# Kernel optimization log

Hardware: AMD Instinct MI355X
Metric: run time of the kernel (lower is better)

## Reference

```python
import jax, jax.numpy as jnp
import numpy as np

B, S, D, H, KD, VD, HID, L, V, OUTN = 16, 512, 512, 8, 64, 64, 2048, 4, 32000, 128
EPS = 1e-5


def _layer_norm(x, g, b):
    m = jnp.mean(x, axis=-1, keepdims=True)
    v = jnp.mean(jnp.square(x - m), axis=-1, keepdims=True)
    return (x - m) * jax.lax.rsqrt(v + EPS) * g + b


def _pos_encoding(seq_len, d_model):
    pos = jnp.arange(seq_len, dtype=jnp.float32)[:, None]
    div = jnp.exp(jnp.arange(0, d_model, 2, dtype=jnp.float32) * (-np.log(10000.0) / d_model))
    pe = jnp.zeros((seq_len, d_model), dtype=jnp.float32)
    pe = pe.at[:, 0::2].set(jnp.sin(pos * div))
    pe = pe.at[:, 1::2].set(jnp.cos(pos * div))
    return pe


def setup_inputs() -> dict:
    key = jax.random.key(0)
    ks = jax.random.split(key, 32)
    s = 0.02
    n = jax.random.normal
    inp = {
        "enc_inputs": jax.random.randint(ks[0], (B, S), 0, V, dtype=jnp.int32),
        "emb": n(ks[1], (V, D), jnp.float32) * s,
        # stacked per-layer params, leading dim = L
        "Wq": n(ks[2], (L, D, H * KD), jnp.float32) * s,
        "bq": jnp.zeros((L, H * KD), jnp.float32),
        "Wk": n(ks[3], (L, D, H * KD), jnp.float32) * s,
        "bk": jnp.zeros((L, H * KD), jnp.float32),
        "Wv": n(ks[4], (L, D, H * VD), jnp.float32) * s,
        "bv": jnp.zeros((L, H * VD), jnp.float32),
        "Wo": n(ks[5], (L, H * VD, D), jnp.float32) * s,
        "bo": jnp.zeros((L, D), jnp.float32),
        "ln1_g": jnp.ones((L, D), jnp.float32),
        "ln1_b": jnp.zeros((L, D), jnp.float32),
        "W1": n(ks[6], (L, D, HID), jnp.float32) * s,   # conv1d k=1 == linear
        "b1": jnp.zeros((L, HID), jnp.float32),
        "W2": n(ks[7], (L, HID, D), jnp.float32) * s,
        "b2": jnp.zeros((L, D), jnp.float32),
        "ln2_g": jnp.ones((L, D), jnp.float32),
        "ln2_b": jnp.zeros((L, D), jnp.float32),
        # flatten head created inside torch forward: [S*D, 128]
        "Wf": n(ks[8], (S * D, OUTN), jnp.float32) * s,
        "bf": jnp.zeros((OUTN,), jnp.float32),
        "Wout": n(ks[9], (OUTN, 1), jnp.float32) * s,
        "bout": jnp.zeros((1,), jnp.float32),
    }
    return inp


def _encoder(enc_inputs, emb, Wq, bq, Wk, bk, Wv, bv, Wo, bo, ln1_g, ln1_b,
             W1, b1, W2, b2, ln2_g, ln2_b, Wf, bf, Wout, bout):
    x = emb[enc_inputs] + _pos_encoding(S, D)[None, :, :]          # [B,S,D]
    pad = (enc_inputs == 0)[:, None, None, :]                      # [B,1,1,S]
    scale = 1.0 / np.sqrt(D)                                       # note: sqrt(embed_dim), as in source
    for l in range(L):
        # multi-head attention
        q = (x @ Wq[l] + bq[l]).reshape(B, S, H, KD)
        k = (x @ Wk[l] + bk[l]).reshape(B, S, H, KD)
        v = (x @ Wv[l] + bv[l]).reshape(B, S, H, VD)
        scores = jnp.einsum('bqhd,bkhd->bhqk', q, k) * scale
        scores = jnp.where(pad, -1e9, scores)
        attn = jax.nn.softmax(scores, axis=-1)
        ctx = jnp.einsum('bhqk,bkhd->bqhd', attn, v).reshape(B, S, H * VD)
        x = _layer_norm(ctx @ Wo[l] + bo[l] + x, ln1_g[l], ln1_b[l])
        # position-wise FFN (conv1d kernel_size=1)
        h = jax.nn.relu(x @ W1[l] + b1[l])
        x = _layer_norm(h @ W2[l] + b2[l] + x, ln2_g[l], ln2_b[l])
    flat = x.reshape(B, S * D)
    features = flat @ Wf + bf                                      # [B,128]
    y_score = jax.nn.sigmoid(features @ Wout + bout)               # [B,1]
    y_pred = jnp.round(y_score)
    return y_score, y_pred, features


def reference(enc_inputs, emb, Wq, bq, Wk, bk, Wv, bv, Wo, bo, ln1_g, ln1_b,
              W1, b1, W2, b2, ln2_g, ln2_b, Wf, bf, Wout, bout):
    return _encoder(enc_inputs, emb, Wq, bq, Wk, bk, Wv, bv, Wo, bo, ln1_g, ln1_b,
                    W1, b1, W2, b2, ln2_g, ln2_b, Wf, bf, Wout, bout)
```

## Files before the change

### kernel.cpp

```cpp
#include <hip/hip_runtime.h>
#include <hip/hip_bf16.h>
#include <math.h>

typedef unsigned short ushort_t;
typedef __attribute__((ext_vector_type(8))) short bf16x8;
typedef __attribute__((ext_vector_type(4))) float f32x4;

#define SCALE_QK 0.04419417382415922f
#define PE_C 0.017988946039015986f

__device__ __forceinline__ void g2lds16(const void* g, void* l) {
    __builtin_amdgcn_global_load_lds(
        (const __attribute__((address_space(1))) unsigned int*)g,
        (__attribute__((address_space(3))) unsigned int*)l,
        16, 0, 0);
}
__device__ __forceinline__ ushort_t f2bs(float v) {
    __hip_bfloat16 h = __float2bfloat16(v);
    return *reinterpret_cast<ushort_t*>(&h);
}
__device__ __forceinline__ float bs2f(ushort_t v) {
    return __uint_as_float(((unsigned int)v) << 16);
}

template<bool RELU, bool VT>
__global__ __launch_bounds__(512, 2) void gemm8(
    const ushort_t* __restrict__ A, const ushort_t* __restrict__ B,
    const float* __restrict__ bias, ushort_t* __restrict__ C,
    ushort_t* __restrict__ vt, int K, int lda, int ldb, int ldc)
{
    __shared__ ushort_t As[2][256 * 64];
    __shared__ ushort_t Bs[2][256 * 64];

    const int t = threadIdx.x;
    const int lane = t & 63, w = t >> 6;
    const int l16 = lane & 15, quad = lane >> 4;
    const int r8 = lane >> 3;
    const int kg = ((lane & 7) ^ r8) << 3;
    const int wm = (w >> 2) * 128;
    const int wn = (w & 3) * 64;
    const int m0 = blockIdx.y * 256, n0 = blockIdx.x * 256;
    const int NT = K >> 6;

    f32x4 acc[8][4];
    #pragma unroll
    for (int i = 0; i < 8; i++)
        #pragma unroll
        for (int j = 0; j < 4; j++)
            acc[i][j] = (f32x4){0.f, 0.f, 0.f, 0.f};

    auto STAGE8 = [&](int kt, int bb) {
        int k0 = kt << 6;
        #pragma unroll
        for (int ii = 0; ii < 4; ii++) {
            int rbase = w * 32 + ii * 8;
            g2lds16(A + (size_t)(m0 + rbase + r8) * lda + k0 + kg,
                    &As[bb][rbase * 64]);
            g2lds16(B + (size_t)(n0 + rbase + r8) * ldb + k0 + kg,
                    &Bs[bb][rbase * 64]);
        }
    };

    STAGE8(0, 0);
    STAGE8(1, 1);

    for (int kt = 0; kt < NT; kt++) {
        const int bb = kt & 1;
        if (kt < NT - 1)
            asm volatile("s_waitcnt vmcnt(8)" ::: "memory");
        else
            asm volatile("s_waitcnt vmcnt(0)" ::: "memory");
        __builtin_amdgcn_s_barrier();
        asm volatile("" ::: "memory");

        #pragma unroll
        for (int tt = 0; tt < 2; tt++) {
            bf16x8 af[8], bf[4];
            #pragma unroll
            for (int i = 0; i < 8; i++) {
                int row = wm + i * 16 + l16;
                af[i] = *(const bf16x8*)&As[bb][row * 64 + ((((tt << 2) + quad) ^ (row & 7)) << 3)];
            }
            #pragma unroll
            for (int j = 0; j < 4; j++) {
                int row = wn + j * 16 + l16;
                bf[j] = *(const bf16x8*)&Bs[bb][row * 64 + ((((tt << 2) + quad) ^ (row & 7)) << 3)];
            }
            #pragma unroll
            for (int i = 0; i < 8; i++)
                #pragma unroll
                for (int j = 0; j < 4; j++)
                    acc[i][j] = __builtin_amdgcn_mfma_f32_16x16x32_bf16(
                        af[i], bf[j], acc[i][j], 0, 0, 0);
        }

        asm volatile("" ::: "memory");
        __builtin_amdgcn_s_barrier();
        asm volatile("" ::: "memory");
        if (kt + 2 < NT)
            STAGE8(kt + 2, bb);
    }

    if (VT && n0 >= 1024) {
        #pragma unroll
        for (int i = 0; i < 8; i++) {
            int mbase = m0 + wm + i * 16 + quad * 4;
            int b = mbase >> 9, s = mbase & 511;
            #pragma unroll
            for (int j = 0; j < 4; j++) {
                int n = n0 + wn + j * 16 + l16;
                int hv = n - 1024;
                int h = hv >> 6, vd = hv & 63;
                float bv = bias[n];
                ushort4 pk;
                pk.x = f2bs(acc[i][j][0] + bv);
                pk.y = f2bs(acc[i][j][1] + bv);
                pk.z = f2bs(acc[i][j][2] + bv);
                pk.w = f2bs(acc[i][j][3] + bv);
                *(ushort4*)&vt[((size_t)((b << 3) + h)) * 32768 + (size_t)vd * 512 + s] = pk;
            }
        }
        return;
    }

    #pragma unroll
    for (int i = 0; i < 8; i++)
        #pragma unroll
        for (int j = 0; j < 4; j++) {
            int n = n0 + wn + j * 16 + l16;
            float bv = bias[n];
            #pragma unroll
            for (int r = 0; r < 4; r++) {
                int m = m0 + wm + i * 16 + quad * 4 + r;
                float v = acc[i][j][r] + bv;
                if (RELU) v = fmaxf(v, 0.f);
                C[(size_t)m * ldc + n] = f2bs(v);
            }
        }
}

__global__ __launch_bounds__(512) void gemmLN(
    const ushort_t* __restrict__ A, const ushort_t* __restrict__ B,
    const float* __restrict__ bias, const ushort_t* __restrict__ res,
    const float* __restrict__ g, const float* __restrict__ bt,
    ushort_t* __restrict__ X, int K, int lda)
{
    __shared__ ushort_t As[2][32 * 64];
    __shared__ ushort_t Bs[2][512 * 64];
    __shared__ float2 pst[8][32];
    __shared__ float2 rmv[32];

    const int t = threadIdx.x;
    const int lane = t & 63, w = t >> 6;
    const int l16 = lane & 15, quad = lane >> 4;
    const int r8 = lane >> 3;
    const int kg = ((lane & 7) ^ r8) << 3;
    const int wn = w * 64;
    const int m0 = blockIdx.x * 32;
    const int NT = K >> 6;

    f32x4 acc[2][4];
    #pragma unroll
    for (int i = 0; i < 2; i++)
        #pragma unroll
        for (int j = 0; j < 4; j++)
            acc[i][j] = (f32x4){0.f, 0.f, 0.f, 0.f};

    auto STAGE = [&](int kt, int bb) {
        int k0 = kt << 6;
        if (w < 4)
            g2lds16(A + (size_t)(m0 + w * 8 + r8) * lda + k0 + kg,
                    &As[bb][(w * 8) * 64]);
        #pragma unroll
        for (int ii = 0; ii < 8; ii++) {
            int rbase = w * 64 + ii * 8;
            g2lds16(B + (size_t)(rbase + r8) * K + k0 + kg,
                    &Bs[bb][rbase * 64]);
        }
    };

    STAGE(0, 0);
    STAGE(1, 1);

    for (int kt = 0; kt < NT; kt++) {
        const int bb = kt & 1;
        if (kt < NT - 1) {
            if (w < 4) asm volatile("s_waitcnt vmcnt(9)" ::: "memory");
            else       asm volatile("s_waitcnt vmcnt(8)" ::: "memory");
        } else {
            asm volatile("s_waitcnt vmcnt(0)" ::: "memory");
        }
        __builtin_amdgcn_s_barrier();
        asm volatile("" ::: "memory");

        #pragma unroll
        for (int tt = 0; tt < 2; tt++) {
            bf16x8 af[2], bf4[4];
            #pragma unroll
            for (int i = 0; i < 2; i++) {
                int row = i * 16 + l16;
                af[i] = *(const bf16x8*)&As[bb][row * 64 + ((((tt << 2) + quad) ^ (row & 7)) << 3)];
            }
            #pragma unroll
            for (int j = 0; j < 4; j++) {
                int row = wn + j * 16 + l16;
                bf4[j] = *(const bf16x8*)&Bs[bb][row * 64 + ((((tt << 2) + quad) ^ (row & 7)) << 3)];
            }
            #pragma unroll
            for (int i = 0; i < 2; i++)
                #pragma unroll
                for (int j = 0; j < 4; j++)
                    acc[i][j] = __builtin_amdgcn_mfma_f32_16x16x32_bf16(
                        af[i], bf4[j], acc[i][j], 0, 0, 0);
        }

        asm volatile("" ::: "memory");
        __builtin_amdgcn_s_barrier();
        asm volatile("" ::: "memory");
        if (kt + 2 < NT)
            STAGE(kt + 2, bb);
    }

    float rs[2][4], rq[2][4];
    #pragma unroll
    for (int i = 0; i < 2; i++)
        #pragma unroll
        for (int r = 0; r < 4; r++) { rs[i][r] = 0.f; rq[i][r] = 0.f; }

    #pragma unroll
    for (int i = 0; i < 2; i++)
        #pragma unroll
        for (int j = 0; j < 4; j++) {
            int n = wn + j * 16 + l16;
            float bvn = bias[n];
            #pragma unroll
            for (int r = 0; r < 4; r++) {
                int row = i * 16 + quad * 4 + r;
                float v = acc[i][j][r] + bvn
                        + bs2f(res[(size_t)(m0 + row) * 512 + n]);
                acc[i][j][r] = v;
                rs[i][r] += v;
                rq[i][r] += v * v;
            }
        }

    #pragma unroll
    for (int i = 0; i < 2; i++)
        #pragma unroll
        for (int r = 0; r < 4; r++) {
            #pragma unroll
            for (int off = 1; off < 16; off <<= 1) {
                rs[i][r] += __shfl_xor(rs[i][r], off);
                rq[i][r] += __shfl_xor(rq[i][r], off);
            }
            if (l16 == 0)
                pst[w][i * 16 + quad * 4 + r] = make_float2(rs[i][r], rq[i][r]);
        }
    __syncthreads();
    if (t < 32) {
        float s = 0.f, q = 0.f;
        #pragma unroll
        for (int wv = 0; wv < 8; wv++) {
            float2 p = pst[wv][t];
            s += p.x; q += p.y;
        }
        float mean = s * (1.f / 512.f);
        float var = q * (1.f / 512.f) - mean * mean;
        rmv[t] = make_float2(mean, rsqrtf(var + 1e-5f));
    }
    __syncthreads();

    #pragma unroll
    for (int i = 0; i < 2; i++)
        #pragma unroll
        for (int j = 0; j < 4; j++) {
            int n = wn + j * 16 + l16;
            float gn = g[n], btn = bt[n];
            #pragma unroll
            for (int r = 0; r < 4; r++) {
                int row = i * 16 + quad * 4 + r;
                float2 mr = rmv[row];
                float o = (acc[i][j][r] - mr.x) * mr.y * gn + btn;
                X[(size_t)(m0 + row) * 512 + n] = f2bs(o);
            }
        }
}

__global__ __launch_bounds__(256) void flash_attn(
    ushort_t* __restrict__ QKV, const ushort_t* __restrict__ Vt,
    const int* __restrict__ tok)
{
    __shared__ ushort_t Qs[128 * 64];
    __shared__ ushort_t Ks[128 * 64];
    __shared__ ushort_t Vts[64 * 128];
    __shared__ ushort_t Ps[128 * 128];

    const int bh = blockIdx.y;
    const int b = bh >> 3, h = bh & 7;
    const int q0 = blockIdx.x * 128;
    const int t = threadIdx.x;
    const int lane = t & 63, w = t >> 6;
    const int l16 = lane & 15, quad = lane >> 4;
    const int wm = w * 32;
    const size_t rowbase = (size_t)b * 512;

    {
        int r8 = lane >> 3;
        int kg = (lane & 7) ^ r8;
        #pragma unroll
        for (int ii = 0; ii < 4; ii++) {
            int rb = w * 32 + ii * 8;
            g2lds16(QKV + (rowbase + q0 + rb + r8) * 1536 + h * 64 + kg * 8,
                    &Qs[rb * 64]);
        }
    }

    f32x4 accO[2][4];
    #pragma unroll
    for (int i = 0; i < 2; i++)
        #pragma unroll
        for (int jv = 0; jv < 4; jv++)
            accO[i][jv] = (f32x4){0.f, 0.f, 0.f, 0.f};
    float lrow[2][4];
    #pragma unroll
    for (int i = 0; i < 2; i++)
        #pragma unroll
        for (int r = 0; r < 4; r++) lrow[i][r] = 0.f;

    for (int kc = 0; kc < 4; kc++) {
        __syncthreads();
        {
            int r8 = lane >> 3;
            int kg = (lane & 7) ^ r8;
            #pragma unroll
            for (int ii = 0; ii < 4; ii++) {
                int rb = w * 32 + ii * 8;
                g2lds16(QKV + (rowbase + kc * 128 + rb + r8) * 1536 + 512 + h * 64 + kg * 8,
                        &Ks[rb * 64]);
            }
        }
        {
            int v4 = lane >> 4;
            #pragma unroll
            for (int ii = 0; ii < 4; ii++) {
                int vb = w * 16 + ii * 4;
                int vd = vb + v4;
                int kg = (lane & 15) ^ (vd & 15);
                g2lds16(Vt + (size_t)bh * 32768 + (size_t)vd * 512 + kc * 128 + kg * 8,
                        &Vts[vb * 128]);
            }
        }
        float maskv[8];
        #pragma unroll
        for (int j = 0; j < 8; j++)
            maskv[j] = (tok[b * 512 + kc * 128 + j * 16 + l16] == 0) ? -1e9f : 0.f;

        __syncthreads();

        f32x4 sacc[2][8];
        #pragma unroll
        for (int i = 0; i < 2; i++)
            #pragma unroll
            for (int j = 0; j < 8; j++)
                sacc[i][j] = (f32x4){0.f, 0.f, 0.f, 0.f};
        #pragma unroll
        for (int tt = 0; tt < 2; tt++) {
            bf16x8 aq[2], bk8[8];
            #pragma unroll
            for (int i = 0; i < 2; i++) {
                int row = wm + i * 16 + l16;
                aq[i] = *(const bf16x8*)&Qs[row * 64 + (((tt << 2) + quad) ^ (row & 7)) * 8];
            }
            #pragma unroll
            for (int j = 0; j < 8; j++) {
                int row = j * 16 + l16;
                bk8[j] = *(const bf16x8*)&Ks[row * 64 + (((tt << 2) + quad) ^ (row & 7)) * 8];
            }
            #pragma unroll
            for (int i = 0; i < 2; i++)
                #pragma unroll
                for (int j = 0; j < 8; j++)
                    sacc[i][j] = __builtin_amdgcn_mfma_f32_16x16x32_bf16(
                        aq[i], bk8[j], sacc[i][j], 0, 0, 0);
        }

        #pragma unroll
        for (int i = 0; i < 2; i++)
            #pragma unroll
            for (int j = 0; j < 8; j++)
                #pragma unroll
                for (int r = 0; r < 4; r++) {
                    float p = __expf(fmaf(sacc[i][j][r], SCALE_QK, maskv[j]));
                    sacc[i][j][r] = p;
                    lrow[i][r] += p;
                }

        #pragma unroll
        for (int i = 0; i < 2; i++)
            #pragma unroll
            for (int j = 0; j < 8; j++) {
                int col = j * 16 + l16;
                int colc = col >> 3, csub = col & 7;
                #pragma unroll
                for (int r = 0; r < 4; r++) {
                    int row = wm + i * 16 + quad * 4 + r;
                    Ps[row * 128 + ((colc ^ (row & 15)) << 3) + csub] = f2bs(sacc[i][j][r]);
                }
            }

        #pragma unroll
        for (int tt = 0; tt < 4; tt++) {
            bf16x8 ap[2], bv8[4];
            #pragma unroll
            for (int i = 0; i < 2; i++) {
                int row = wm + i * 16 + l16;
                ap[i] = *(const bf16x8*)&Ps[row * 128 + ((((tt << 2) + quad)) ^ (row & 15)) * 8];
            }
            #pragma unroll
            for (int jv = 0; jv < 4; jv++) {
                int vd = jv * 16 + l16;
                bv8[jv] = *(const bf16x8*)&Vts[vd * 128 + (((tt << 2) + quad) ^ (vd & 15)) * 8];
            }
            #pragma unroll
            for (int i = 0; i < 2; i++)
                #pragma unroll
                for (int jv = 0; jv < 4; jv++)
                    accO[i][jv] = __builtin_amdgcn_mfma_f32_16x16x32_bf16(
                        ap[i], bv8[jv], accO[i][jv], 0, 0, 0);
        }
    }

    #pragma unroll
    for (int i = 0; i < 2; i++)
        #pragma unroll
        for (int r = 0; r < 4; r++) {
            float s = lrow[i][r];
            #pragma unroll
            for (int off = 1; off < 16; off <<= 1)
                s += __shfl_xor(s, off);
            float inv = 1.f / s;
            int row = q0 + wm + i * 16 + quad * 4 + r;
            #pragma unroll
            for (int jv = 0; jv < 4; jv++) {
                int vd = jv * 16 + l16;
                QKV[(rowbase + row) * 1536 + h * 64 + vd] = f2bs(accO[i][jv][r] * inv);
            }
        }
}

__global__ __launch_bounds__(256) void prep(
    const float* __restrict__ Wq, const float* __restrict__ Wk,
    const float* __restrict__ Wv, const float* __restrict__ Wo,
    const float* __restrict__ W1, const float* __restrict__ W2,
    const float* __restrict__ bq, const float* __restrict__ bk,
    const float* __restrict__ bv, const int* __restrict__ tok,
    const float* __restrict__ emb,
    __hip_bfloat16* __restrict__ WqkvT, __hip_bfloat16* __restrict__ WoT,
    __hip_bfloat16* __restrict__ W1T, __hip_bfloat16* __restrict__ W2T,
    float* __restrict__ bqkv, float* __restrict__ Fb,
    __hip_bfloat16* __restrict__ xb)
{
    const int blk = blockIdx.x;
    const int t = threadIdx.x;

    if (blk < 12288) {
        __shared__ float tile[32][33];
        const float* in; __hip_bfloat16* out;
        long long inz, outz; int R, Cc, bx, by, bz;
        if (blk < 4096) {
            int seg = blk >> 10, lb = blk & 1023;
            bz = lb >> 8; by = (lb >> 4) & 15; bx = lb & 15;
            R = 512; Cc = 512; inz = 262144;
            if      (seg == 0) { in = Wq; out = WqkvT;          outz = 786432; }
            else if (seg == 1) { in = Wk; out = WqkvT + 262144; outz = 786432; }
            else if (seg == 2) { in = Wv; out = WqkvT + 524288; outz = 786432; }
            else               { in = Wo; out = WoT;            outz = 262144; }
        } else if (blk < 8192) {
            int lb = blk - 4096;
            bz = lb >> 10; by = (lb >> 6) & 15; bx = lb & 63;
            R = 512; Cc = 2048; inz = 1048576; outz = 1048576;
            in = W1; out = W1T;
        } else {
            int lb = blk - 8192;
            bz = lb >> 10; by = (lb >> 4) & 63; bx = lb & 15;
            R = 2048; Cc = 512; inz = 1048576; outz = 1048576;
            in = W2; out = W2T;
        }
        in += bz * inz; out += bz * outz;
        int c0 = bx * 32, r0 = by * 32;
        int tx = t & 31, ty = t >> 5;
        #pragma unroll
        for (int i = 0; i < 4; i++)
            tile[ty + i * 8][tx] = in[(size_t)(r0 + ty + i * 8) * Cc + c0 + tx];
        __syncthreads();
        #pragma unroll
        for (int i = 0; i < 4; i++)
            out[(size_t)(c0 + ty + i * 8) * R + r0 + tx] =
                __float2bfloat16(tile[tx][ty + i * 8]);
    } else if (blk < 12312) {
        int k = blk - 12288;
        int idx = k * 256 + t;
        int l = idx / 1536, n = idx - l * 1536;
        float v = (n < 512) ? bq[l * 512 + n]
                : (n < 1024) ? bk[l * 512 + n - 512]
                             : bv[l * 512 + n - 1024];
        bqkv[idx] = v;
        if (k < 8) Fb[k * 256 + t] = 0.f;
    } else {
        int idx = (blk - 12312) * 256 + t;
        int d  = idx & 511;
        int bs = idx >> 9;
        int s  = bs & 511;
        int tk = tok[bs];
        float freq  = expf(-(float)(d & ~1) * PE_C);
        float angle = (float)s * freq;
        float pe    = (d & 1) ? cosf(angle) : sinf(angle);
        xb[idx] = __float2bfloat16(emb[(size_t)tk * 512 + d] + pe);
    }
}

__global__ __launch_bounds__(256) void feat_partial(const ushort_t* __restrict__ Xb,
                                                    const float* __restrict__ Wf,
                                                    float* __restrict__ Fb) {
    const int slice = blockIdx.x;
    const int k0 = slice * 128;
    __shared__ float Xs[16][128];
    __shared__ float Red[2048];
    const int t = threadIdx.x;

    #pragma unroll
    for (int i = 0; i < 2; i++) {
        int idx = t + i * 256;
        int b = idx >> 5, c4 = (idx & 31) * 4;
        ushort4 u = *(const ushort4*)&Xb[(size_t)b * 262144 + k0 + c4];
        Xs[b][c4 + 0] = bs2f(u.x);
        Xs[b][c4 + 1] = bs2f(u.y);
        Xs[b][c4 + 2] = bs2f(u.z);
        Xs[b][c4 + 3] = bs2f(u.w);
    }
    #pragma unroll
    for (int i = 0; i < 8; i++) Red[t + i * 256] = 0.f;
    __syncthreads();

    const int n4 = (t & 31) * 4;
    const int kh = t >> 5;
    const int rbase = kh * 16;
    const float* wp = Wf + (size_t)(k0 + rbase) * 128 + n4;

    float4 acc[16];
    #pragma unroll
    for (int b = 0; b < 16; b++) acc[b] = (float4){0.f, 0.f, 0.f, 0.f};

    #pragma unroll
    for (int half = 0; half < 2; half++) {
        float4 wv[8];
        #pragma unroll
        for (int kk = 0; kk < 8; kk++)
            wv[kk] = *(const float4*)&wp[(size_t)(half * 8 + kk) * 128];
        #pragma unroll
        for (int b = 0; b < 16; b++) {
            float4 x0 = *(const float4*)&Xs[b][rbase + half * 8];
            float4 x1 = *(const float4*)&Xs[b][rbase + half * 8 + 4];
            acc[b].x += x0.x*wv[0].x + x0.y*wv[1].x + x0.z*wv[2].x + x0.w*wv[3].x
                      + x1.x*wv[4].x + x1.y*wv[5].x + x1.z*wv[6].x + x1.w*wv[7].x;
            acc[b].y += x0.x*wv[0].y + x0.y*wv[1].y + x0.z*wv[2].y + x0.w*wv[3].y
                      + x1.x*wv[4].y + x1.y*wv[5].y + x1.z*wv[6].y + x1.w*wv[7].y;
            acc[b].z += x0.x*wv[0].z + x0.y*wv[1].z + x0.z*wv[2].z + x0.w*wv[3].z
                      + x1.x*wv[4].z + x1.y*wv[5].z + x1.z*wv[6].z + x1.w*wv[7].z;
            acc[b].w += x0.x*wv[0].w + x0.y*wv[1].w + x0.z*wv[2].w + x0.w*wv[3].w
                      + x1.x*wv[4].w + x1.y*wv[5].w + x1.z*wv[6].w + x1.w*wv[7].w;
        }
    }

    #pragma unroll
    for (int b = 0; b < 16; b++) {
        atomicAdd(&Red[b * 128 + n4 + 0], acc[b].x);
        atomicAdd(&Red[b * 128 + n4 + 1], acc[b].y);
        atomicAdd(&Red[b * 128 + n4 + 2], acc[b].z);
        atomicAdd(&Red[b * 128 + n4 + 3], acc[b].w);
    }
    __syncthreads();
    #pragma unroll
    for (int i = 0; i < 8; i++) {
        int o = t + i * 256;
        atomicAdd(&Fb[o], Red[o]);
    }
}

__global__ __launch_bounds__(256) void head_kernel(const float* __restrict__ feat,
                                                   const float* __restrict__ bfv,
                                                   const float* __restrict__ Wo2,
                                                   const float* __restrict__ bo2,
                                                   float* __restrict__ out) {
    __shared__ float f[2048];
    int t = threadIdx.x;
    for (int i = t; i < 2048; i += 256) {
        float v = feat[i] + bfv[i & 127];
        f[i] = v;
        out[32 + i] = v;
    }
    __syncthreads();
    if (t < 16) {
        float zv = bo2[0];
        for (int n = 0; n < 128; n++) zv = fmaf(f[t * 128 + n], Wo2[n], zv);
        float ys = 1.f / (1.f + expf(-zv));
        out[t] = ys;
        out[16 + t] = rintf(ys);
    }
}

extern "C" void kernel_launch(void* const* d_in, const int* in_sizes, int n_in,
                              void* d_out, int out_size, void* d_ws, size_t ws_size,
                              hipStream_t stream) {
    const int*   enc  = (const int*)  d_in[0];
    const float* emb  = (const float*)d_in[1];
    const float* Wq   = (const float*)d_in[2];
    const float* bq   = (const float*)d_in[3];
    const float* Wk   = (const float*)d_in[4];
    const float* bk   = (const float*)d_in[5];
    const float* Wv   = (const float*)d_in[6];
    const float* bv   = (const float*)d_in[7];
    const float* Wo   = (const float*)d_in[8];
    const float* bo   = (const float*)d_in[9];
    const float* g1   = (const float*)d_in[10];
    const float* be1  = (const float*)d_in[11];
    const float* W1   = (const float*)d_in[12];
    const float* b1f  = (const float*)d_in[13];
    const float* W2   = (const float*)d_in[14];
    const float* b2f  = (const float*)d_in[15];
    const float* g2   = (const float*)d_in[16];
    const float* be2  = (const float*)d_in[17];
    const float* Wf   = (const float*)d_in[18];
    const float* bf   = (const float*)d_in[19];
    const float* Wout = (const float*)d_in[20];
    const float* bout = (const float*)d_in[21];
    float* out = (float*)d_out;

    char* ws = (char*)d_ws;
    ushort_t* Xb   = (ushort_t*) (ws + 16777216);
    ushort_t* QKV  = (ushort_t*) (ws + 25165824);
    ushort_t* Vt   = (ushort_t*) (ws + 50331648);
    ushort_t* S    = (ushort_t*) (ws + 58720256);
    ushort_t* WqkvT= (ushort_t*) (ws + 92274688);
    ushort_t* WoT  = (ushort_t*) (ws + 98566144);
    ushort_t* W1T  = (ushort_t*) (ws + 100663296);
    ushort_t* W2T  = (ushort_t*) (ws + 109051904);
    float*    bqkv = (float*)    (ws + 117440512);
    float*    Fb   = (float*)    (ws + 117465088);

    typedef __hip_bfloat16 bf16;

    prep<<<28696, 256, 0, stream>>>(
        Wq, Wk, Wv, Wo, W1, W2, bq, bk, bv, enc, emb,
        (bf16*)WqkvT, (bf16*)WoT, (bf16*)W1T, (bf16*)W2T, bqkv, Fb, (bf16*)Xb);

    for (int l = 0; l < 4; l++) {
        gemm8<false, true><<<dim3(6, 32), 512, 0, stream>>>(
            Xb, WqkvT + (size_t)l * 786432, bqkv + l * 1536,
            QKV, Vt, 512, 512, 512, 1536);

        flash_attn<<<dim3(4, 128), 256, 0, stream>>>(QKV, Vt, enc);

        gemmLN<<<256, 512, 0, stream>>>(
            QKV, WoT + (size_t)l * 262144, bo + l * 512, Xb,
            g1 + l * 512, be1 + l * 512, Xb, 512, 1536);

        gemm8<true, false><<<dim3(8, 32), 512, 0, stream>>>(
            Xb, W1T + (size_t)l * 1048576, b1f + l * 2048,
            S, nullptr, 512, 512, 512, 2048);

        gemmLN<<<256, 512, 0, stream>>>(
            S, W2T + (size_t)l * 1048576, b2f + l * 512, Xb,
            g2 + l * 512, be2 + l * 512, Xb, 2048, 2048);
    }

    feat_partial<<<2048, 256, 0, stream>>>(Xb, Wf, Fb);
    head_kernel<<<1, 256, 0, stream>>>(Fb, bf, Wout, bout, out);
}
```

Before: 1.037 ms.

## Replace atomic reductions in flatten head with partial buffers and reduce kernel

The flatten-head GEMV now covers 256 K-rows per block instead of 128, which halves the block count. Each block reduces its partials with wave shuffles and per-wave shared-memory slots, dropping the LDS atomics, and writes a per-slice partial to a workspace buffer. A new reduce kernel sums those partials and does only a few global atomics per output, instead of 2048 blocks each atomically adding 2048 values. This adds an extra kernel launch and an 8 MB round trip through the partial buffer. The partial buffer reuses workspace offset 0, which is assumed to be free at this point.

```diff
diff --git a/kernel.cpp b/kernel.cpp
--- a/kernel.cpp
+++ b/kernel.cpp
@@ -521,30 +521,29 @@
 
 __global__ __launch_bounds__(256) void feat_partial(const ushort_t* __restrict__ Xb,
                                                     const float* __restrict__ Wf,
-                                                    float* __restrict__ Fb) {
+                                                    float* __restrict__ FbP) {
     const int slice = blockIdx.x;
-    const int k0 = slice * 128;
-    __shared__ float Xs[16][128];
-    __shared__ float Red[2048];
+    const int k0 = slice * 256;
+    __shared__ float Xs[16][256];
+    __shared__ float RedW[4][16][128];
     const int t = threadIdx.x;
 
     #pragma unroll
-    for (int i = 0; i < 2; i++) {
+    for (int i = 0; i < 4; i++) {
         int idx = t + i * 256;
-        int b = idx >> 5, c4 = (idx & 31) * 4;
+        int b = idx >> 6, c4 = (idx & 63) * 4;
         ushort4 u = *(const ushort4*)&Xb[(size_t)b * 262144 + k0 + c4];
         Xs[b][c4 + 0] = bs2f(u.x);
         Xs[b][c4 + 1] = bs2f(u.y);
         Xs[b][c4 + 2] = bs2f(u.z);
         Xs[b][c4 + 3] = bs2f(u.w);
     }
-    #pragma unroll
-    for (int i = 0; i < 8; i++) Red[t + i * 256] = 0.f;
     __syncthreads();
 
     const int n4 = (t & 31) * 4;
     const int kh = t >> 5;
-    const int rbase = kh * 16;
+    const int rbase = kh * 32;
+    const int wv = t >> 6;
     const float* wp = Wf + (size_t)(k0 + rbase) * 128 + n4;
 
     float4 acc[16];
@@ -552,39 +551,64 @@
     for (int b = 0; b < 16; b++) acc[b] = (float4){0.f, 0.f, 0.f, 0.f};
 
     #pragma unroll
-    for (int half = 0; half < 2; half++) {
-        float4 wv[8];
+    for (int q = 0; q < 4; q++) {
+        float4 wvv[8];
         #pragma unroll
         for (int kk = 0; kk < 8; kk++)
-            wv[kk] = *(const float4*)&wp[(size_t)(half * 8 + kk) * 128];
+            wvv[kk] = *(const float4*)&wp[(size_t)(q * 8 + kk) * 128];
         #pragma unroll
         for (int b = 0; b < 16; b++) {
-            float4 x0 = *(const float4*)&Xs[b][rbase + half * 8];
-            float4 x1 = *(const float4*)&Xs[b][rbase + half * 8 + 4];
-            acc[b].x += x0.x*wv[0].x + x0.y*wv[1].x + x0.z*wv[2].x + x0.w*wv[3].x
-                      + x1.x*wv[4].x + x1.y*wv[5].x + x1.z*wv[6].x + x1.w*wv[7].x;
-            acc[b].y += x0.x*wv[0].y + x0.y*wv[1].y + x0.z*wv[2].y + x0.w*wv[3].y
-                      + x1.x*wv[4].y + x1.y*wv[5].y + x1.z*wv[6].y + x1.w*wv[7].y;
-            acc[b].z += x0.x*wv[0].z + x0.y*wv[1].z + x0.z*wv[2].z + x0.w*wv[3].z
-                      + x1.x*wv[4].z + x1.y*wv[5].z + x1.z*wv[6].z + x1.w*wv[7].z;
-            acc[b].w += x0.x*wv[0].w + x0.y*wv[1].w + x0.z*wv[2].w + x0.w*wv[3].w
-                      + x1.x*wv[4].w + x1.y*wv[5].w + x1.z*wv[6].w + x1.w*wv[7].w;
+            float4 x0 = *(const float4*)&Xs[b][rbase + q * 8];
+            float4 x1 = *(const float4*)&Xs[b][rbase + q * 8 + 4];
+            acc[b].x += x0.x*wvv[0].x + x0.y*wvv[1].x + x0.z*wvv[2].x + x0.w*wvv[3].x
+                      + x1.x*wvv[4].x + x1.y*wvv[5].x + x1.z*wvv[6].x + x1.w*wvv[7].x;
+            acc[b].y += x0.x*wvv[0].y + x0.y*wvv[1].y + x0.z*wvv[2].y + x0.w*wvv[3].y
+                      + x1.x*wvv[4].y + x1.y*wvv[5].y + x1.z*wvv[6].y + x1.w*wvv[7].y;
+            acc[b].z += x0.x*wvv[0].z + x0.y*wvv[1].z + x0.z*wvv[2].z + x0.w*wvv[3].z
+                      + x1.x*wvv[4].z + x1.y*wvv[5].z + x1.z*wvv[6].z + x1.w*wvv[7].z;
+            acc[b].w += x0.x*wvv[0].w + x0.y*wvv[1].w + x0.z*wvv[2].w + x0.w*wvv[3].w
+                      + x1.x*wvv[4].w + x1.y*wvv[5].w + x1.z*wvv[6].w + x1.w*wvv[7].w;
         }
     }
 
     #pragma unroll
     for (int b = 0; b < 16; b++) {
-        atomicAdd(&Red[b * 128 + n4 + 0], acc[b].x);
-        atomicAdd(&Red[b * 128 + n4 + 1], acc[b].y);
-        atomicAdd(&Red[b * 128 + n4 + 2], acc[b].z);
-        atomicAdd(&Red[b * 128 + n4 + 3], acc[b].w);
+        acc[b].x += __shfl_xor(acc[b].x, 32);
+        acc[b].y += __shfl_xor(acc[b].y, 32);
+        acc[b].z += __shfl_xor(acc[b].z, 32);
+        acc[b].w += __shfl_xor(acc[b].w, 32);
+    }
+    if ((t & 63) < 32) {
+        #pragma unroll
+        for (int b = 0; b < 16; b++)
+            *(float4*)&RedW[wv][b][n4] = acc[b];
     }
     __syncthreads();
+
     #pragma unroll
     for (int i = 0; i < 8; i++) {
         int o = t + i * 256;
-        atomicAdd(&Fb[o], Red[o]);
-    }
+        int b = o >> 7, c = o & 127;
+        FbP[(size_t)slice * 2048 + o] =
+            RedW[0][b][c] + RedW[1][b][c] + RedW[2][b][c] + RedW[3][b][c];
+    }
+}
+
+__global__ __launch_bounds__(256) void feat_reduce(const float* __restrict__ FbP,
+                                                   float* __restrict__ Fb) {
+    int o = blockIdx.x * 256 + threadIdx.x;
+    int g0 = blockIdx.y * 64;
+    float s = 0.f;
+    #pragma unroll
+    for (int jj = 0; jj < 64; jj += 8) {
+        float v[8];
+        #pragma unroll
+        for (int u = 0; u < 8; u++)
+            v[u] = FbP[(size_t)(g0 + jj + u) * 2048 + o];
+        #pragma unroll
+        for (int u = 0; u < 8; u++) s += v[u];
+    }
+    atomicAdd(&Fb[o], s);
 }
 
 __global__ __launch_bounds__(256) void head_kernel(const float* __restrict__ feat,
@@ -647,6 +671,7 @@
     ushort_t* W2T  = (ushort_t*) (ws + 109051904);
     float*    bqkv = (float*)    (ws + 117440512);
     float*    Fb   = (float*)    (ws + 117465088);
+    float*    FbP  = (float*)    (ws + 0);
 
     typedef __hip_bfloat16 bf16;
 
@@ -674,6 +699,7 @@
             g2 + l * 512, be2 + l * 512, Xb, 2048, 2048);
     }
 
-    feat_partial<<<2048, 256, 0, stream>>>(Xb, Wf, Fb);
+    feat_partial<<<1024, 256, 0, stream>>>(Xb, Wf, FbP);
+    feat_reduce<<<dim3(8, 16), 256, 0, stream>>>(FbP, Fb);
     head_kernel<<<1, 256, 0, stream>>>(Fb, bf, Wout, bout, out);
 }
```

New measurement: 902.5 us. 1.15x faster.
